# Performance work log

Measured on AMD Instinct MI355X. Metric: run time of the kernel, lower is better.

Reference implementation:

```python
import jax, jax.numpy as jnp
import numpy as np

N_CLASSES = 80
TOPK = 13
ALPHA = 1.0
BETA = 6.0
EPS = 1e-9
BS, N_ANCHORS, N_MAX = 32, 8400, 100


def setup_inputs() -> dict:
    key = jax.random.key(0)
    k1, k2, k3, k4, k5, k6 = jax.random.split(key, 6)
    pred_scores = jax.random.uniform(k1, (BS, N_ANCHORS, N_CLASSES), dtype=jnp.float32)
    anchor_points = jax.random.uniform(k2, (N_ANCHORS, 2), dtype=jnp.float32) * 640.0
    # predicted boxes centered on anchor points (valid xyxy)
    wh = jax.random.uniform(k3, (BS, N_ANCHORS, 2), dtype=jnp.float32) * 100.0 + 4.0
    ctr = anchor_points[None]
    pred_bboxes = jnp.concatenate([ctr - wh / 2, ctr + wh / 2], axis=-1)
    gt_lt = jax.random.uniform(k4, (BS, N_MAX, 2), dtype=jnp.float32) * 500.0
    gt_wh = jax.random.uniform(k5, (BS, N_MAX, 2), dtype=jnp.float32) * 120.0 + 8.0
    gt_bboxes = jnp.concatenate([gt_lt, gt_lt + gt_wh], axis=-1)
    gt_labels = jax.random.randint(k6, (BS, N_MAX, 1), 0, N_CLASSES).astype(jnp.int32)
    mask_gt = jnp.ones((BS, N_MAX, 1), dtype=jnp.float32)
    return {"pred_scores": pred_scores, "pred_bboxes": pred_bboxes,
            "anchor_points": anchor_points, "gt_labels": gt_labels,
            "gt_bboxes": gt_bboxes, "mask_gt": mask_gt}


def _batch_iou(a, b):
    # a: [bs, n, 4], b: [bs, m, 4] (xyxy) -> [bs, n, m]
    lt = jnp.maximum(a[:, :, None, :2], b[:, None, :, :2])
    rb = jnp.minimum(a[:, :, None, 2:], b[:, None, :, 2:])
    wh = jnp.clip(rb - lt, 0.0)
    inter = wh[..., 0] * wh[..., 1]
    area_a = ((a[..., 2] - a[..., 0]) * (a[..., 3] - a[..., 1]))[:, :, None]
    area_b = ((b[..., 2] - b[..., 0]) * (b[..., 3] - b[..., 1]))[:, None, :]
    return inter / (area_a + area_b - inter + EPS)


def _assign(pred_scores, pred_bboxes, anchor_points, gt_labels, gt_bboxes, mask_gt):
    bs, n_anchors, n_classes = pred_scores.shape
    n_max = gt_bboxes.shape[1]
    labels = gt_labels[..., 0].astype(jnp.int32)  # [bs, n_max]

    # alignment metric: bbox_scores[b,g,a] = pred_scores[b,a,labels[b,g]]
    ps_t = jnp.swapaxes(pred_scores, 1, 2)  # [bs, C, n_anchors]
    bbox_scores = jnp.take_along_axis(ps_t, labels[:, :, None], axis=1)  # [bs, n_max, n_anchors]
    overlaps = _batch_iou(gt_bboxes, pred_bboxes)  # [bs, n_max, n_anchors]
    align_metric = jnp.power(bbox_scores, ALPHA) * jnp.power(overlaps, BETA)

    # anchor centers inside gt boxes
    ap = anchor_points[None, None, :, :]  # [1,1,n_anchors,2]
    deltas = jnp.concatenate(
        [ap - gt_bboxes[:, :, None, :2], gt_bboxes[:, :, None, 2:] - ap], axis=-1)
    is_in_gts = (deltas.min(axis=-1) > EPS).astype(align_metric.dtype)  # [bs,n_max,n_anchors]

    # topk candidate selection
    metrics = align_metric * is_in_gts
    _, topk_idxs = jax.lax.top_k(metrics, TOPK)  # [bs, n_max, TOPK]
    topk_mask = (mask_gt > 0)  # [bs, n_max, 1], broadcasts over TOPK
    topk_idxs = jnp.where(topk_mask, topk_idxs, 0)

    def count_row(idx):  # idx: [TOPK] -> anchor hit counts [n_anchors]
        return jnp.zeros((n_anchors,), jnp.int32).at[idx].add(1)
    counts = jax.vmap(jax.vmap(count_row))(topk_idxs)  # [bs, n_max, n_anchors]
    is_in_topk = jnp.where(counts > 1, 0, counts).astype(metrics.dtype)

    mask_pos = is_in_topk * is_in_gts * mask_gt  # [bs, n_max, n_anchors]

    # fix collisions: anchors assigned to multiple GTs keep the max-IoU GT
    mask_pos_sum = mask_pos.sum(axis=1)  # [bs, n_anchors]
    multi = mask_pos_sum[:, None, :] > 1
    is_max_overlaps = jax.nn.one_hot(overlaps.argmax(axis=1), n_max, axis=1,
                                     dtype=mask_pos.dtype)  # [bs, n_max, n_anchors]
    mask_pos = jnp.where(multi, is_max_overlaps, mask_pos)
    mask_pos_sum = mask_pos.sum(axis=1)
    assigned_gt_idx = mask_pos.argmax(axis=1)  # [bs, n_anchors]

    # final assignments via flattened gather
    flat_idx = assigned_gt_idx + jnp.arange(bs, dtype=jnp.int32)[:, None] * n_max
    assigned_labels = labels.reshape(-1)[flat_idx]  # [bs, n_anchors]
    assigned_bboxes = gt_bboxes.reshape(-1, 4)[flat_idx]  # [bs, n_anchors, 4]
    assigned_labels = jnp.where(assigned_labels < 0, 0, assigned_labels)
    assigned_scores = jax.nn.one_hot(assigned_labels, n_classes, dtype=pred_scores.dtype)
    pos = mask_pos_sum > 0
    assigned_scores = jnp.where(pos[..., None], assigned_scores, 0.0)
    assigned_labels = jnp.where(pos, assigned_labels, n_classes)

    # normalize scores by alignment metric
    align_metric = align_metric * mask_pos
    pos_align = align_metric.max(axis=-1, keepdims=True)  # [bs, n_max, 1]
    pos_overlaps = (overlaps * mask_pos).max(axis=-1, keepdims=True)
    norm = (align_metric * pos_overlaps / (pos_align + EPS)).max(axis=1)[..., None]  # [bs,n_anchors,1]
    assigned_scores = assigned_scores * norm

    return assigned_labels, assigned_bboxes, assigned_scores, pos


def reference(pred_scores, pred_bboxes, anchor_points, gt_labels, gt_bboxes, mask_gt):
    return _assign(pred_scores, pred_bboxes, anchor_points, gt_labels, gt_bboxes, mask_gt)
```

## Files before the change

### kernel.cpp

```cpp
#include <hip/hip_runtime.h>

#define BS 32
#define NA 8400
#define NMAX 100
#define NC 80
#define TOPK 13
#define EPSF 1e-9f
#define CAP 1024
#define NSTRIP 64
#define STRIP_INV 0.1f

#define OFF_LBL  0
#define OFF_BOX  (BS*NA)
#define OFF_SCR  (BS*NA + BS*NA*4)
#define OFF_POS  (BS*NA + BS*NA*4 + BS*NA*NC)

__device__ __forceinline__ float iou_fn(float gx1, float gy1, float gx2, float gy2,
                                        float px1, float py1, float px2, float py2) {
    float lx = fmaxf(gx1, px1), ly = fmaxf(gy1, py1);
    float rx = fminf(gx2, px2), ry = fminf(gy2, py2);
    float w = fmaxf(rx - lx, 0.f), h = fmaxf(ry - ly, 0.f);
    float inter = w * h;
    float aa = (gx2 - gx1) * (gy2 - gy1);
    float ab = (px2 - px1) * (py2 - py1);
    return inter / (aa + ab - inter + EPSF);
}

__global__ __launch_bounds__(256) void bin_kernel(
    const float* __restrict__ anchor_points,
    int* __restrict__ strip_off, float2* __restrict__ sAP, int* __restrict__ sIdx)
{
    __shared__ int cnt[NSTRIP];
    __shared__ int cur[NSTRIP];
    int t = threadIdx.x;
    if (t < NSTRIP) cnt[t] = 0;
    __syncthreads();
    const float2* ap2 = (const float2*)anchor_points;
    for (int a = t; a < NA; a += 256) {
        int s = (int)(ap2[a].y * STRIP_INV);
        s = s < 0 ? 0 : (s > NSTRIP - 1 ? NSTRIP - 1 : s);
        atomicAdd(&cnt[s], 1);
    }
    __syncthreads();
    if (t == 0) {
        int acc = 0;
        for (int s = 0; s < NSTRIP; s++) {
            cur[s] = acc; strip_off[s] = acc; acc += cnt[s];
        }
        strip_off[NSTRIP] = acc;
    }
    __syncthreads();
    for (int a = t; a < NA; a += 256) {
        float2 p = ap2[a];
        int s = (int)(p.y * STRIP_INV);
        s = s < 0 ? 0 : (s > NSTRIP - 1 ? NSTRIP - 1 : s);
        int pos = atomicAdd(&cur[s], 1);
        sAP[pos] = p;
        sIdx[pos] = a;
    }
}

__global__ __launch_bounds__(256) void topk_kernel(
    const float* __restrict__ pred_scores,
    const float* __restrict__ pred_bboxes,
    const int*   __restrict__ gt_labels,
    const float* __restrict__ gt_bboxes,
    const float* __restrict__ mask_gt,
    const int*   __restrict__ strip_off,
    const float2* __restrict__ sAP,
    const int*   __restrict__ sIdx,
    unsigned int* __restrict__ claims)
{
    int row = blockIdx.x;
    int b = row / NMAX, j = row % NMAX;
    if (mask_gt[row] <= 0.f) return;

    __shared__ unsigned long long cand[CAP];
    __shared__ unsigned short aidx[CAP];
    __shared__ int ncand;

    int t = threadIdx.x;
    if (t == 0) ncand = 0;
    __syncthreads();

    const float* gb = gt_bboxes + (size_t)row * 4;
    float gx1 = gb[0], gy1 = gb[1], gx2 = gb[2], gy2 = gb[3];
    int lab = gt_labels[row];

    int s_lo = (int)(gy1 * STRIP_INV); s_lo = s_lo < 0 ? 0 : (s_lo > NSTRIP-1 ? NSTRIP-1 : s_lo);
    int s_hi = (int)(gy2 * STRIP_INV); s_hi = s_hi < 0 ? 0 : (s_hi > NSTRIP-1 ? NSTRIP-1 : s_hi);
    int lo = strip_off[s_lo], hi = strip_off[s_hi + 1];

    int lane = t & 63;
    for (int base = lo; base < hi; base += 256) {
        int p = base + t;
        bool hit = false;
        int a = 0;
        if (p < hi) {
            float2 ap = sAP[p];
            a = sIdx[p];
            hit = (ap.x - gx1 > EPSF) && (ap.y - gy1 > EPSF) &&
                  (gx2 - ap.x > EPSF) && (gy2 - ap.y > EPSF);
        }
        unsigned long long m = __ballot(hit);
        if (m != 0ULL) {
            int basepos = 0;
            if (lane == 0) basepos = atomicAdd(&ncand, __popcll(m));
            basepos = __shfl(basepos, 0, 64);
            if (hit) {
                int my = basepos + __popcll(m & ((1ULL << lane) - 1ULL));
                if (my < CAP) aidx[my] = (unsigned short)a;
            }
        }
    }
    __syncthreads();
    int n = ncand < CAP ? ncand : CAP;

    const float4* pb4 = (const float4*)pred_bboxes;
    for (int p = t; p < n; p += 256) {
        int a = aidx[p];
        float4 pb = pb4[b * NA + a];
        float iou = iou_fn(gx1, gy1, gx2, gy2, pb.x, pb.y, pb.z, pb.w);
        float s = pred_scores[((size_t)b * NA + a) * NC + lab];
        float i2 = iou * iou;
        float m = s * (i2 * i2 * i2);
        cand[p] = (m > 0.f)
                    ? (((unsigned long long)__float_as_uint(m) << 32) |
                       (unsigned int)(NA - a))
                    : 0ULL;
    }
    __syncthreads();

    if (t >= 64) return;

    unsigned long long loc[TOPK];
    #pragma unroll
    for (int i = 0; i < TOPK; i++) loc[i] = 0ULL;
    for (int p = t; p < n; p += 64) {
        unsigned long long k = cand[p];
        #pragma unroll
        for (int i = 0; i < TOPK; i++) {
            if (k > loc[i]) { unsigned long long tmp = loc[i]; loc[i] = k; k = tmp; }
        }
    }

    int head = 0;
    for (int r = 0; r < TOPK; r++) {
        unsigned long long h = (head < TOPK) ? loc[head] : 0ULL;
        unsigned long long m = h;
        #pragma unroll
        for (int s = 32; s > 0; s >>= 1) {
            unsigned long long o = __shfl_xor(m, s, 64);
            m = o > m ? o : m;
        }
        if (m == 0ULL) break;
        unsigned long long ball = __ballot(h == m);
        int winner = (int)__builtin_ctzll(ball);
        if (t == winner) {
            head++;
            int a = NA - (int)(unsigned int)(m & 0xFFFFFFFFULL);
            atomicAdd(&claims[b * NA + a], (1u << 16) | (unsigned int)j);
        }
    }
}

__global__ __launch_bounds__(256) void resolve_kernel(
    const float* __restrict__ pred_scores,
    const float* __restrict__ pred_bboxes,
    const int*   __restrict__ gt_labels,
    const float* __restrict__ gt_bboxes,
    const unsigned int* __restrict__ claims,
    int* __restrict__ assigned_j, float* __restrict__ a_align,
    unsigned int* __restrict__ pa_bits, unsigned int* __restrict__ po_bits)
{
    __shared__ float4 gtb[NMAX];
    __shared__ int    glab[NMAX];
    int b = blockIdx.y;
    int t = threadIdx.x;
    if (t < NMAX) {
        gtb[t]  = ((const float4*)gt_bboxes)[b * NMAX + t];
        glab[t] = gt_labels[b * NMAX + t];
    }
    __syncthreads();

    int ai = blockIdx.x * 256 + t;
    if (ai >= NA) return;
    int idx = b * NA + ai;
    unsigned int pk = claims[idx];
    if (pk == 0u) { assigned_j[idx] = -1; a_align[idx] = 0.f; return; }

    float4 pb = ((const float4*)pred_bboxes)[idx];

    int js;
    if ((pk >> 16) == 1u) {
        js = (int)(pk & 0xFFFFu);
    } else {
        float best = -1.f; js = 0;
        for (int j = 0; j < NMAX; j++) {
            float4 g = gtb[j];
            float v = iou_fn(g.x, g.y, g.z, g.w, pb.x, pb.y, pb.z, pb.w);
            if (v > best) { best = v; js = j; }
        }
    }
    float4 g = gtb[js];
    float iou = iou_fn(g.x, g.y, g.z, g.w, pb.x, pb.y, pb.z, pb.w);
    int lab = glab[js];
    float s = pred_scores[(size_t)idx * NC + lab];
    float i2 = iou * iou;
    float align = s * (i2 * i2 * i2);
    assigned_j[idx] = js; a_align[idx] = align;
    atomicMax(&pa_bits[b * NMAX + js], __float_as_uint(align));
    atomicMax(&po_bits[b * NMAX + js], __float_as_uint(iou));
}

__global__ __launch_bounds__(256) void finalize_kernel(
    const int*   __restrict__ gt_labels,
    const float* __restrict__ gt_bboxes,
    const int* __restrict__ assigned_j,
    const float* __restrict__ a_align,
    const unsigned int* __restrict__ pa_bits, const unsigned int* __restrict__ po_bits,
    float* __restrict__ out)
{
    int t = threadIdx.x;
    int idx = blockIdx.x * 256 + t;
    int b = idx / NA;
    int js = assigned_j[idx];
    bool pos = js >= 0;
    int j0 = pos ? js : 0;
    int lab = gt_labels[b * NMAX + j0];

    out[OFF_LBL + idx] = pos ? (float)lab : (float)NC;

    float4 gb = ((const float4*)gt_bboxes)[b * NMAX + j0];
    ((float4*)(out + OFF_BOX))[idx] = gb;

    out[OFF_POS + idx] = pos ? 1.f : 0.f;

    float4* sc = (float4*)(out + OFF_SCR + (size_t)blockIdx.x * 256 * NC);
    float4 z = make_float4(0.f, 0.f, 0.f, 0.f);
    #pragma unroll
    for (int i = 0; i < 256 * NC / 4 / 256; i++)
        sc[t + i * 256] = z;
    __syncthreads();

    if (pos) {
        float pa = __uint_as_float(pa_bits[b * NMAX + js]);
        float po = __uint_as_float(po_bits[b * NMAX + js]);
        float norm = a_align[idx] * po / (pa + EPSF);
        out[OFF_SCR + (size_t)idx * NC + lab] = norm;
    }
}

extern "C" void kernel_launch(void* const* d_in, const int* in_sizes, int n_in,
                              void* d_out, int out_size, void* d_ws, size_t ws_size,
                              hipStream_t stream) {
    const float* pred_scores   = (const float*)d_in[0];
    const float* pred_bboxes   = (const float*)d_in[1];
    const float* anchor_points = (const float*)d_in[2];
    const int*   gt_labels     = (const int*)d_in[3];
    const float* gt_bboxes     = (const float*)d_in[4];
    const float* mask_gt       = (const float*)d_in[5];

    char* ws = (char*)d_ws;
    const size_t NBA = (size_t)BS * NA;
    unsigned int* claims   = (unsigned int*)(ws);
    unsigned int* pa_bits  = (unsigned int*)(ws + NBA * 4);
    unsigned int* po_bits  = (unsigned int*)(ws + NBA * 4 + (size_t)BS * NMAX * 4);
    int*   assigned_j = (int*)(ws + NBA * 4 + (size_t)BS * NMAX * 8);
    float* a_align    = (float*)(ws + NBA * 8 + (size_t)BS * NMAX * 8);
    size_t off5 = NBA * 12 + (size_t)BS * NMAX * 8;
    int*    strip_off = (int*)(ws + off5);
    float2* sAP       = (float2*)(ws + off5 + 512);
    int*    sIdx      = (int*)(ws + off5 + 512 + (size_t)NA * 8);

    float* out = (float*)d_out;

    hipMemsetAsync(claims, 0, NBA * 4 + (size_t)BS * NMAX * 8, stream);

    bin_kernel<<<1, 256, 0, stream>>>(anchor_points, strip_off, sAP, sIdx);

    topk_kernel<<<BS * NMAX, 256, 0, stream>>>(
        pred_scores, pred_bboxes, gt_labels, gt_bboxes, mask_gt,
        strip_off, sAP, sIdx, claims);

    dim3 rgrid((NA + 255) / 256, BS);
    resolve_kernel<<<rgrid, 256, 0, stream>>>(
        pred_scores, pred_bboxes, gt_labels, gt_bboxes, claims,
        assigned_j, a_align, pa_bits, po_bits);

    finalize_kernel<<<(int)(NBA / 256), 256, 0, stream>>>(
        gt_labels, gt_bboxes, assigned_j, a_align, pa_bits, po_bits, out);
}
```

Measured before the change: 243.8 us.

## Map one GT row per wavefront in topk kernel and parallelize strip scan

The top-k kernel now processes four GT rows per block, one per 64-lane wavefront. Each wave compacts candidates with a ballot-based running count instead of a shared atomic, and folds the IoU/score computation straight into the per-lane top-13 insertion. This removes the block-wide __syncthreads and the 64-bit candidate shared array, at the cost of fewer lanes working on each row. The binning kernel moves to 1024 threads and replaces its serial prefix sum with a wave shuffle scan.

```diff
diff --git a/kernel.cpp b/kernel.cpp
--- a/kernel.cpp
+++ b/kernel.cpp
@@ -6,7 +6,7 @@
 #define NC 80
 #define TOPK 13
 #define EPSF 1e-9f
-#define CAP 1024
+#define WCAP 1024
 #define NSTRIP 64
 #define STRIP_INV 0.1f
 
@@ -26,7 +26,7 @@
     return inter / (aa + ab - inter + EPSF);
 }
 
-__global__ __launch_bounds__(256) void bin_kernel(
+__global__ __launch_bounds__(1024) void bin_kernel(
     const float* __restrict__ anchor_points,
     int* __restrict__ strip_off, float2* __restrict__ sAP, int* __restrict__ sIdx)
 {
@@ -36,21 +36,26 @@
     if (t < NSTRIP) cnt[t] = 0;
     __syncthreads();
     const float2* ap2 = (const float2*)anchor_points;
-    for (int a = t; a < NA; a += 256) {
+    for (int a = t; a < NA; a += 1024) {
         int s = (int)(ap2[a].y * STRIP_INV);
         s = s < 0 ? 0 : (s > NSTRIP - 1 ? NSTRIP - 1 : s);
         atomicAdd(&cnt[s], 1);
     }
     __syncthreads();
-    if (t == 0) {
-        int acc = 0;
-        for (int s = 0; s < NSTRIP; s++) {
-            cur[s] = acc; strip_off[s] = acc; acc += cnt[s];
-        }
-        strip_off[NSTRIP] = acc;
-    }
-    __syncthreads();
-    for (int a = t; a < NA; a += 256) {
+    if (t < 64) {
+        int v = cnt[t];
+        int inc = v;
+        #pragma unroll
+        for (int d = 1; d < 64; d <<= 1) {
+            int o = __shfl_up(inc, d, 64);
+            if (t >= d) inc += o;
+        }
+        int excl = inc - v;
+        cur[t] = excl; strip_off[t] = excl;
+        if (t == 63) strip_off[64] = inc;
+    }
+    __syncthreads();
+    for (int a = t; a < NA; a += 1024) {
         float2 p = ap2[a];
         int s = (int)(p.y * STRIP_INV);
         s = s < 0 ? 0 : (s > NSTRIP - 1 ? NSTRIP - 1 : s);
@@ -71,82 +76,64 @@
     const int*   __restrict__ sIdx,
     unsigned int* __restrict__ claims)
 {
-    int row = blockIdx.x;
+    __shared__ unsigned short aidx[4][WCAP];
+    int wave = threadIdx.x >> 6;
+    int lane = threadIdx.x & 63;
+    int row = blockIdx.x * 4 + wave;
     int b = row / NMAX, j = row % NMAX;
     if (mask_gt[row] <= 0.f) return;
 
-    __shared__ unsigned long long cand[CAP];
-    __shared__ unsigned short aidx[CAP];
-    __shared__ int ncand;
-
-    int t = threadIdx.x;
-    if (t == 0) ncand = 0;
-    __syncthreads();
-
-    const float* gb = gt_bboxes + (size_t)row * 4;
-    float gx1 = gb[0], gy1 = gb[1], gx2 = gb[2], gy2 = gb[3];
+    const float* gbp = gt_bboxes + (size_t)row * 4;
+    float gx1 = gbp[0], gy1 = gbp[1], gx2 = gbp[2], gy2 = gbp[3];
     int lab = gt_labels[row];
 
     int s_lo = (int)(gy1 * STRIP_INV); s_lo = s_lo < 0 ? 0 : (s_lo > NSTRIP-1 ? NSTRIP-1 : s_lo);
     int s_hi = (int)(gy2 * STRIP_INV); s_hi = s_hi < 0 ? 0 : (s_hi > NSTRIP-1 ? NSTRIP-1 : s_hi);
     int lo = strip_off[s_lo], hi = strip_off[s_hi + 1];
 
-    int lane = t & 63;
-    for (int base = lo; base < hi; base += 256) {
-        int p = base + t;
-        bool hit = false;
-        int a = 0;
+    int cnt = 0;
+    for (int base = lo; base < hi; base += 64) {
+        int p = base + lane;
+        bool hit = false; int a = 0;
         if (p < hi) {
             float2 ap = sAP[p];
             a = sIdx[p];
             hit = (ap.x - gx1 > EPSF) && (ap.y - gy1 > EPSF) &&
                   (gx2 - ap.x > EPSF) && (gy2 - ap.y > EPSF);
         }
-        unsigned long long m = __ballot(hit);
-        if (m != 0ULL) {
-            int basepos = 0;
-            if (lane == 0) basepos = atomicAdd(&ncand, __popcll(m));
-            basepos = __shfl(basepos, 0, 64);
-            if (hit) {
-                int my = basepos + __popcll(m & ((1ULL << lane) - 1ULL));
-                if (my < CAP) aidx[my] = (unsigned short)a;
-            }
-        }
-    }
-    __syncthreads();
-    int n = ncand < CAP ? ncand : CAP;
-
-    const float4* pb4 = (const float4*)pred_bboxes;
-    for (int p = t; p < n; p += 256) {
-        int a = aidx[p];
-        float4 pb = pb4[b * NA + a];
-        float iou = iou_fn(gx1, gy1, gx2, gy2, pb.x, pb.y, pb.z, pb.w);
-        float s = pred_scores[((size_t)b * NA + a) * NC + lab];
-        float i2 = iou * iou;
-        float m = s * (i2 * i2 * i2);
-        cand[p] = (m > 0.f)
-                    ? (((unsigned long long)__float_as_uint(m) << 32) |
-                       (unsigned int)(NA - a))
-                    : 0ULL;
-    }
-    __syncthreads();
-
-    if (t >= 64) return;
+        unsigned long long mb = __ballot(hit);
+        if (hit) {
+            int my = cnt + __popcll(mb & ((1ULL << lane) - 1ULL));
+            if (my < WCAP) aidx[wave][my] = (unsigned short)a;
+        }
+        cnt += __popcll(mb);
+    }
+    if (cnt > WCAP) cnt = WCAP;
 
     unsigned long long loc[TOPK];
     #pragma unroll
     for (int i = 0; i < TOPK; i++) loc[i] = 0ULL;
-    for (int p = t; p < n; p += 64) {
-        unsigned long long k = cand[p];
-        #pragma unroll
-        for (int i = 0; i < TOPK; i++) {
-            if (k > loc[i]) { unsigned long long tmp = loc[i]; loc[i] = k; k = tmp; }
-        }
-    }
-
-    int head = 0;
+    const float4* pb4 = (const float4*)pred_bboxes;
+    for (int p = lane; p < cnt; p += 64) {
+        int a = aidx[wave][p];
+        float4 pb = pb4[b * NA + a];
+        float s = pred_scores[((size_t)b * NA + a) * NC + lab];
+        float iou = iou_fn(gx1, gy1, gx2, gy2, pb.x, pb.y, pb.z, pb.w);
+        float i2 = iou * iou;
+        float m = s * (i2 * i2 * i2);
+        if (m > 0.f) {
+            unsigned long long key =
+                ((unsigned long long)__float_as_uint(m) << 32) |
+                (unsigned int)(NA - a);
+            #pragma unroll
+            for (int i = 0; i < TOPK; i++) {
+                if (key > loc[i]) { unsigned long long tmp = loc[i]; loc[i] = key; key = tmp; }
+            }
+        }
+    }
+
     for (int r = 0; r < TOPK; r++) {
-        unsigned long long h = (head < TOPK) ? loc[head] : 0ULL;
+        unsigned long long h = loc[0];
         unsigned long long m = h;
         #pragma unroll
         for (int s = 32; s > 0; s >>= 1) {
@@ -155,9 +142,10 @@
         }
         if (m == 0ULL) break;
         unsigned long long ball = __ballot(h == m);
-        int winner = (int)__builtin_ctzll(ball);
-        if (t == winner) {
-            head++;
+        if (lane == (int)__builtin_ctzll(ball)) {
+            #pragma unroll
+            for (int i = 0; i < TOPK - 1; i++) loc[i] = loc[i + 1];
+            loc[TOPK - 1] = 0ULL;
             int a = NA - (int)(unsigned int)(m & 0xFFFFFFFFULL);
             atomicAdd(&claims[b * NA + a], (1u << 16) | (unsigned int)j);
         }
@@ -277,9 +265,9 @@
 
     hipMemsetAsync(claims, 0, NBA * 4 + (size_t)BS * NMAX * 8, stream);
 
-    bin_kernel<<<1, 256, 0, stream>>>(anchor_points, strip_off, sAP, sIdx);
-
-    topk_kernel<<<BS * NMAX, 256, 0, stream>>>(
+    bin_kernel<<<1, 1024, 0, stream>>>(anchor_points, strip_off, sAP, sIdx);
+
+    topk_kernel<<<BS * NMAX / 4, 256, 0, stream>>>(
         pred_scores, pred_bboxes, gt_labels, gt_bboxes, mask_gt,
         strip_off, sAP, sIdx, claims);
 
```

Result: faster. 233.6 us (-4.2%).
